# Optimization experiments

Measured on AMD Instinct MI355X. Metric: run time of the kernel, lower is better.

## Reference

```python
import jax, jax.numpy as jnp
import numpy as np

C, KT, D, De, Df, H, PH = 2048, 64, 1024, 128, 256, 8, 1024


def setup_inputs() -> dict:
    key = jax.random.key(0)
    ks = jax.random.split(key, 10)
    wscale = lambda k, shape: jax.random.normal(k, shape, jnp.float32) * 0.02
    return {
        "w": jax.random.normal(ks[0], (C, D), jnp.float32),
        "F": jax.random.normal(ks[1], (C, KT, D), jnp.float32),
        "Et": jax.random.normal(ks[2], (C, KT, De), jnp.float32),
        "fC": jax.random.normal(ks[3], (C, Df), jnp.float32),
        "W1": wscale(ks[4], (D, D + De)),   # K proj (out, in), Linear weight layout
        "W2": wscale(ks[5], (D, D)),        # Q proj
        "Wv": wscale(ks[6], (D, D + De)),   # V proj
        "Wf": wscale(ks[7], (D, Df)),       # fC_proj
        "alpha": jnp.full((1,), 0.1, jnp.float32),
        "beta": jnp.full((1,), 0.1, jnp.float32),
        "g1_w": wscale(ks[8], (PH, D + De)),
        "g1_b": jnp.zeros((PH,), jnp.float32),
        "g2_w": wscale(ks[9], (D, PH)),
        "g2_b": jnp.full((D,), -2.0, jnp.float32),  # bias init fill_(-2.0)
    }


def reference(w, F, Et, fC, W1, W2, Wv, Wf, alpha, beta, g1_w, g1_b, g2_w, g2_b):
    Cc, KTt, Dd = F.shape
    Hh = H
    dh = Dd // Hh
    Fp = jnp.concatenate([F, Et], axis=-1)                 # [C,KT,D+De]
    K = jnp.einsum('ckx,dx->ckd', Fp, W1)                  # [C,KT,D]
    Q = w @ W2.T                                           # [C,D]
    V = jnp.einsum('ckx,dx->ckd', Fp, Wv)                  # [C,KT,D]
    fCp = fC @ Wf.T                                        # [C,D]
    K = K + alpha * fCp[:, None, :]
    Q = Q + beta * fCp
    Qh = Q.reshape(Cc, Hh, dh)                             # [C,H,dh]
    Kh = K.reshape(Cc, KTt, Hh, dh)                        # [C,KT,H,dh]
    Vh = V.reshape(Cc, KTt, Hh, dh)
    scores = jnp.einsum('chd,ckhd->chk', Qh, Kh) / jnp.sqrt(jnp.float32(dh))
    attn = jax.nn.softmax(scores, axis=-1)                 # [C,H,KT]
    A = jnp.einsum('chk,ckhd->chd', attn, Vh).reshape(Cc, Dd)
    gin = jnp.concatenate([w, Et.mean(axis=1)], axis=-1)   # [C,D+De]
    hmid = jax.nn.relu(gin @ g1_w.T + g1_b)
    g = jax.nn.sigmoid(hmid @ g2_w.T + g2_b)               # [C,D] (vec_gate)
    out = w + g * A
    norm = jnp.linalg.norm(out, axis=-1, keepdims=True)
    return out / jnp.maximum(norm, 1e-12)
```

## Files before the change

### kernel.cpp

```cpp
#include <hip/hip_runtime.h>


#define DEV __device__ __forceinline__

typedef __attribute__((ext_vector_type(4))) float f32x4;
typedef __attribute__((ext_vector_type(8))) short bf16x8;
typedef __attribute__((ext_vector_type(4))) unsigned short u16x4;

DEV unsigned short f2b(float f) {
  unsigned int u = __builtin_bit_cast(unsigned int, f);
  u = u + 0x7fffu + ((u >> 16) & 1u);
  return (unsigned short)(u >> 16);
}

enum { MQ = 0, MQT = 1, MAP = 2, MG1 = 3, MG2 = 4 };

template <int MODE>
__global__ __launch_bounds__(256) void gemm64(
    const float* __restrict__ A1, const float* __restrict__ A2,
    const unsigned short* __restrict__ Ab,
    const float* __restrict__ B1, const float* __restrict__ B2,
    const float* __restrict__ scale2, const float* __restrict__ bias,
    float* __restrict__ OutF, unsigned short* __restrict__ OutB)
{
  __shared__ unsigned short As[64 * 40];
  __shared__ unsigned short Bs[64 * 40];

  const int tid = threadIdx.x;
  const int lane = tid & 63, wv = tid >> 6;
  const int l15 = lane & 15, s = lane >> 4;
  const int bx = blockIdx.x, by = blockIdx.y, h = blockIdx.z;
  const int c0 = by * 64;
  const int n0 = bx * 64;

  int K;
  if constexpr (MODE == MQ) K = 1280;
  else if constexpr (MODE == MQT) K = 128;
  else if constexpr (MODE == MAP) K = 1152;
  else if constexpr (MODE == MG1) K = 1152;
  else K = 1024;

  float s2 = 1.0f;
  if constexpr (MODE == MQ) s2 = scale2[0];

  f32x4 acc[4] = {};

  for (int k0 = 0; k0 < K; k0 += 32) {
    if constexpr (MODE == MQ || MODE == MG1) {
      #pragma unroll
      for (int p = 0; p < 2; ++p) {
        int flat = tid + 256 * p;
        int r = flat >> 3, kc = (flat & 7) * 4;
        int k = k0 + kc;
        float4 v;
        if constexpr (MODE == MQ) {
          if (k < 1024) v = *(const float4*)(A1 + (size_t)(c0 + r) * 1024 + k);
          else {
            v = *(const float4*)(A2 + (size_t)(c0 + r) * 256 + (k - 1024));
            v.x *= s2; v.y *= s2; v.z *= s2; v.w *= s2;
          }
        } else {
          if (k < 1024) v = *(const float4*)(A1 + (size_t)(c0 + r) * 1024 + k);
          else v = *(const float4*)(A2 + (size_t)(c0 + r) * 128 + (k - 1024));
        }
        unsigned short* dst = As + r * 40 + kc;
        dst[0] = f2b(v.x); dst[1] = f2b(v.y); dst[2] = f2b(v.z); dst[3] = f2b(v.w);
      }
    } else {
      int r = tid >> 2, kc = (tid & 3) * 8;
      size_t lda, aoff;
      if constexpr (MODE == MQT)      { lda = 1024; aoff = (size_t)h * 128; }
      else if constexpr (MODE == MAP) { lda = 9216; aoff = (size_t)h * 1152; }
      else                            { lda = 1024; aoff = 0; }
      bf16x8 v = *(const bf16x8*)(Ab + (size_t)(c0 + r) * lda + aoff + k0 + kc);
      *(bf16x8*)(As + r * 40 + kc) = v;
    }
    if constexpr (MODE == MQT) {
      #pragma unroll
      for (int p = 0; p < 8; ++p) {
        int flat = tid + 256 * p;
        int kk = flat >> 6, nn = flat & 63;
        float v = B1[(size_t)(h * 128 + k0 + kk) * 1152 + n0 + nn];
        Bs[nn * 40 + kk] = f2b(v);
      }
    } else {
      #pragma unroll
      for (int p = 0; p < 2; ++p) {
        int flat = tid + 256 * p;
        int nn = flat >> 3, kc = (flat & 7) * 4;
        int k = k0 + kc;
        float4 v;
        if constexpr (MODE == MQ) {
          if (k < 1024) v = *(const float4*)(B1 + (size_t)(n0 + nn) * 1024 + k);
          else v = *(const float4*)(B2 + (size_t)(n0 + nn) * 256 + (k - 1024));
        } else if constexpr (MODE == MAP) {
          v = *(const float4*)(B1 + (size_t)(h * 128 + n0 + nn) * 1152 + k);
        } else if constexpr (MODE == MG1) {
          v = *(const float4*)(B1 + (size_t)(n0 + nn) * 1152 + k);
        } else {
          v = *(const float4*)(B1 + (size_t)(n0 + nn) * 1024 + k);
        }
        unsigned short* dst = Bs + nn * 40 + kc;
        dst[0] = f2b(v.x); dst[1] = f2b(v.y); dst[2] = f2b(v.z); dst[3] = f2b(v.w);
      }
    }
    __syncthreads();
    bf16x8 bF = *(const bf16x8*)(Bs + (wv * 16 + l15) * 40 + s * 8);
    #pragma unroll
    for (int ms = 0; ms < 4; ++ms) {
      bf16x8 aF = *(const bf16x8*)(As + (ms * 16 + l15) * 40 + s * 8);
      acc[ms] = __builtin_amdgcn_mfma_f32_16x16x32_bf16(aF, bF, acc[ms], 0, 0, 0);
    }
    __syncthreads();
  }

  #pragma unroll
  for (int ms = 0; ms < 4; ++ms) {
    #pragma unroll
    for (int r = 0; r < 4; ++r) {
      int row = c0 + ms * 16 + s * 4 + r;
      int col = n0 + wv * 16 + l15;
      float v = acc[ms][r];
      if constexpr (MODE == MQ) {
        OutB[(size_t)row * 1024 + col] = f2b(v);
      } else if constexpr (MODE == MQT) {
        OutB[(size_t)row * 9216 + h * 1152 + col] = f2b(v);
      } else if constexpr (MODE == MAP) {
        OutF[(size_t)row * 1024 + h * 128 + col] = v;
      } else if constexpr (MODE == MG1) {
        v += bias[col];
        v = fmaxf(v, 0.0f);
        OutB[(size_t)row * 1024 + col] = f2b(v);
      } else {
        v += bias[col];
        v = 1.0f / (1.0f + __expf(-v));
        OutF[(size_t)row * 1024 + col] = v;
      }
    }
  }
}

__global__ __launch_bounds__(512) void attn_kern(
    const float* __restrict__ F, const float* __restrict__ Et,
    const unsigned short* __restrict__ Qtb,
    unsigned short* __restrict__ Pb, float* __restrict__ Etm)
{
  extern __shared__ char smem[];
  unsigned short* fp = (unsigned short*)smem;
  float* sc = (float*)(smem + (size_t)64 * 1160 * 2);

  const int c = blockIdx.x;
  const int tid = threadIdx.x;
  const int wv = tid >> 6, lane = tid & 63;
  const int l15 = lane & 15, s = lane >> 4;

  const float* Fc = F + (size_t)c * (64 * 1024);
  const float* Ec = Et + (size_t)c * (64 * 128);

  #pragma unroll 4
  for (int j = 0; j < 36; ++j) {
    int i = tid + 512 * j;
    int row = i / 288;
    int c4 = (i % 288) * 4;
    float4 v;
    if (c4 < 1024) v = *(const float4*)(Fc + (size_t)row * 1024 + c4);
    else           v = *(const float4*)(Ec + (size_t)row * 128 + (c4 - 1024));
    u16x4 t4 = { f2b(v.x), f2b(v.y), f2b(v.z), f2b(v.w) };
    *(u16x4*)(fp + (size_t)row * 1160 + c4) = t4;
  }
  __syncthreads();

  if (wv < 4) {
    f32x4 acc = {};
    const unsigned short* qrow = Qtb + ((size_t)c * 8 + l15) * 1152 + s * 8;
    const unsigned short* frow = fp + (size_t)(wv * 16 + l15) * 1160 + s * 8;
    #pragma unroll 4
    for (int x0 = 0; x0 < 1152; x0 += 32) {
      bf16x8 aF = {};
      if (l15 < 8) aF = *(const bf16x8*)(qrow + x0);
      bf16x8 bF = *(const bf16x8*)(frow + x0);
      acc = __builtin_amdgcn_mfma_f32_16x16x32_bf16(aF, bF, acc, 0, 0, 0);
    }
    if (s < 2) {
      #pragma unroll
      for (int r = 0; r < 4; ++r)
        sc[(s * 4 + r) * 64 + wv * 16 + l15] = acc[r] * 0.08838834764831845f;
    }
  } else {
    int u = tid - 256;
    if (u < 128) {
      float ssum = 0.f;
      #pragma unroll 8
      for (int k = 0; k < 64; ++k) ssum += Ec[(size_t)k * 128 + u];
      Etm[(size_t)c * 128 + u] = ssum * (1.0f / 64.0f);
    }
  }
  __syncthreads();

  {
    float sv = sc[wv * 64 + lane];
    float m = sv;
    #pragma unroll
    for (int off = 32; off; off >>= 1) m = fmaxf(m, __shfl_xor(m, off));
    float e = __expf(sv - m);
    float sum = e;
    #pragma unroll
    for (int off = 32; off; off >>= 1) sum += __shfl_xor(sum, off);
    sc[wv * 64 + lane] = e / sum;
  }
  __syncthreads();

  bf16x8 pa[2];
  #pragma unroll
  for (int ki = 0; ki < 2; ++ki) {
    bf16x8 t = {};
    if (l15 < 8) {
      #pragma unroll
      for (int j = 0; j < 8; ++j)
        t[j] = (short)f2b(sc[l15 * 64 + ki * 32 + j * 4 + s]);
    }
    pa[ki] = t;
  }
  #pragma unroll
  for (int ntl = 0; ntl < 9; ++ntl) {
    int nt = wv * 9 + ntl;
    int x = nt * 16 + l15;
    f32x4 acc = {};
    #pragma unroll
    for (int ki = 0; ki < 2; ++ki) {
      bf16x8 bF;
      #pragma unroll
      for (int j = 0; j < 8; ++j)
        bF[j] = (short)fp[(size_t)(ki * 32 + j * 4 + s) * 1160 + x];
      acc = __builtin_amdgcn_mfma_f32_16x16x32_bf16(pa[ki], bF, acc, 0, 0, 0);
    }
    if (s < 2) {
      #pragma unroll
      for (int r = 0; r < 4; ++r) {
        int hh = s * 4 + r;
        Pb[((size_t)c * 8 + hh) * 1152 + x] = f2b(acc[r]);
      }
    }
  }
}

__global__ __launch_bounds__(256) void finalize_kern(
    const float* __restrict__ w, const float* __restrict__ A,
    const float* __restrict__ g, float* __restrict__ out)
{
  __shared__ float red[4];
  int c = blockIdx.x, t = threadIdx.x;
  int lane = t & 63, wid = t >> 6;
  size_t base = (size_t)c * 1024 + t * 4;
  float4 wv = *(const float4*)(w + base);
  float4 av = *(const float4*)(A + base);
  float4 gv = *(const float4*)(g + base);
  float4 o;
  o.x = wv.x + gv.x * av.x;
  o.y = wv.y + gv.y * av.y;
  o.z = wv.z + gv.z * av.z;
  o.w = wv.w + gv.w * av.w;
  float ss = o.x * o.x + o.y * o.y + o.z * o.z + o.w * o.w;
  #pragma unroll
  for (int off = 32; off; off >>= 1) ss += __shfl_xor(ss, off);
  if (lane == 0) red[wid] = ss;
  __syncthreads();
  float tot = red[0] + red[1] + red[2] + red[3];
  float inv = 1.0f / fmaxf(sqrtf(tot), 1e-12f);
  o.x *= inv; o.y *= inv; o.z *= inv; o.w *= inv;
  *(float4*)(out + base) = o;
}

extern "C" void kernel_launch(void* const* d_in, const int* in_sizes, int n_in,
                              void* d_out, int out_size, void* d_ws, size_t ws_size,
                              hipStream_t stream)
{
  (void)in_sizes; (void)n_in; (void)out_size; (void)ws_size;
  const float* w    = (const float*)d_in[0];
  const float* F    = (const float*)d_in[1];
  const float* Et   = (const float*)d_in[2];
  const float* fC   = (const float*)d_in[3];
  const float* W1   = (const float*)d_in[4];
  const float* W2   = (const float*)d_in[5];
  const float* Wv   = (const float*)d_in[6];
  const float* Wf   = (const float*)d_in[7];
  const float* beta = (const float*)d_in[9];
  const float* g1w  = (const float*)d_in[10];
  const float* g1b  = (const float*)d_in[11];
  const float* g2w  = (const float*)d_in[12];
  const float* g2b  = (const float*)d_in[13];
  float* outp = (float*)d_out;

  char* ws = (char*)d_ws;
  unsigned short* Qb  = (unsigned short*)(ws + 0);
  unsigned short* Qtb = (unsigned short*)(ws + 4194304);
  unsigned short* Pb  = (unsigned short*)(ws + 41943040);
  float* Etm          = (float*)(ws + 79691776);
  float* Afp          = (float*)(ws + 80740352);
  unsigned short* Hm  = (unsigned short*)(ws + 4194304);
  float* Gf           = (float*)(ws + 0);

  gemm64<MQ><<<dim3(16, 32), 256, 0, stream>>>(w, fC, nullptr, W2, Wf, beta,
                                               nullptr, nullptr, Qb);
  gemm64<MQT><<<dim3(18, 32, 8), 256, 0, stream>>>(nullptr, nullptr, Qb, W1,
                                                   nullptr, nullptr, nullptr,
                                                   nullptr, Qtb);
  attn_kern<<<2048, 512, 150528, stream>>>(F, Et, Qtb, Pb, Etm);
  gemm64<MAP><<<dim3(2, 32, 8), 256, 0, stream>>>(nullptr, nullptr, Pb, Wv,
                                                  nullptr, nullptr, nullptr,
                                                  Afp, nullptr);
  gemm64<MG1><<<dim3(16, 32), 256, 0, stream>>>(w, Etm, nullptr, g1w, nullptr,
                                                nullptr, g1b, nullptr, Hm);
  gemm64<MG2><<<dim3(16, 32), 256, 0, stream>>>(nullptr, nullptr, Hm, g2w,
                                                nullptr, nullptr, g2b, Gf,
                                                nullptr);
  finalize_kern<<<2048, 256, 0, stream>>>(w, Afp, Gf, outp);
}
```

Before: 1.250 ms.

## Stream attention tiles via async LDS loads with online softmax; widen GEMM K-tile with swizzle

The attention kernel now streams F and Et in four 16-row tiles using global_load_lds into double-buffered fp32 LDS with XOR swizzle. It splits the score reduction across all 8 waves and uses an online softmax with running max and sum rescaling. This is meant to overlap global loads with MFMA work and drop the up-front bulk conversion pass. Separately, the GEMM kernels move to a 64-wide K step with swizzled LDS rows to cut bank conflicts and halve the barrier count. The costs are more LDS (156800 bytes, which rules out two blocks per CU despite the launch bound), per-tile bf16 conversion during compute, and extra synchronization per tile.

```diff
diff --git a/kernel.cpp b/kernel.cpp
--- a/kernel.cpp
+++ b/kernel.cpp
@@ -12,6 +12,26 @@
   u = u + 0x7fffu + ((u >> 16) & 1u);
   return (unsigned short)(u >> 16);
 }
+
+DEV bf16x8 cvt8(f32x4 a, f32x4 b) {
+  bf16x8 r;
+  r[0] = (short)f2b(a[0]); r[1] = (short)f2b(a[1]);
+  r[2] = (short)f2b(a[2]); r[3] = (short)f2b(a[3]);
+  r[4] = (short)f2b(b[0]); r[5] = (short)f2b(b[1]);
+  r[6] = (short)f2b(b[2]); r[7] = (short)f2b(b[3]);
+  return r;
+}
+
+DEV void gll16(const void* g, void* l) {
+  __builtin_amdgcn_global_load_lds(
+      (const __attribute__((address_space(1))) void*)g,
+      (__attribute__((address_space(3))) void*)l, 16, 0, 0);
+}
+
+#define SBAR0() __builtin_amdgcn_sched_barrier(0)
+#define LGKM_BARRIER() do { \
+    asm volatile("s_waitcnt lgkmcnt(0)" ::: "memory"); \
+    SBAR0(); __builtin_amdgcn_s_barrier(); SBAR0(); } while (0)
 
 enum { MQ = 0, MQT = 1, MAP = 2, MG1 = 3, MG2 = 4 };
 
@@ -23,8 +43,8 @@
     const float* __restrict__ scale2, const float* __restrict__ bias,
     float* __restrict__ OutF, unsigned short* __restrict__ OutB)
 {
-  __shared__ unsigned short As[64 * 40];
-  __shared__ unsigned short Bs[64 * 40];
+  __shared__ unsigned short As[64 * 64];
+  __shared__ unsigned short Bs[64 * 64];
 
   const int tid = threadIdx.x;
   const int lane = tid & 63, wv = tid >> 6;
@@ -45,12 +65,12 @@
 
   f32x4 acc[4] = {};
 
-  for (int k0 = 0; k0 < K; k0 += 32) {
+  for (int k0 = 0; k0 < K; k0 += 64) {
     if constexpr (MODE == MQ || MODE == MG1) {
       #pragma unroll
-      for (int p = 0; p < 2; ++p) {
+      for (int p = 0; p < 4; ++p) {
         int flat = tid + 256 * p;
-        int r = flat >> 3, kc = (flat & 7) * 4;
+        int r = flat >> 4, kc = (flat & 15) * 4;
         int k = k0 + kc;
         float4 v;
         if constexpr (MODE == MQ) {
@@ -63,31 +83,35 @@
           if (k < 1024) v = *(const float4*)(A1 + (size_t)(c0 + r) * 1024 + k);
           else v = *(const float4*)(A2 + (size_t)(c0 + r) * 128 + (k - 1024));
         }
-        unsigned short* dst = As + r * 40 + kc;
-        dst[0] = f2b(v.x); dst[1] = f2b(v.y); dst[2] = f2b(v.z); dst[3] = f2b(v.w);
+        u16x4 t4 = { f2b(v.x), f2b(v.y), f2b(v.z), f2b(v.w) };
+        *(u16x4*)((char*)As + r * 128 + ((kc * 2) ^ ((r & 7) << 4))) = t4;
       }
     } else {
-      int r = tid >> 2, kc = (tid & 3) * 8;
-      size_t lda, aoff;
-      if constexpr (MODE == MQT)      { lda = 1024; aoff = (size_t)h * 128; }
-      else if constexpr (MODE == MAP) { lda = 9216; aoff = (size_t)h * 1152; }
-      else                            { lda = 1024; aoff = 0; }
-      bf16x8 v = *(const bf16x8*)(Ab + (size_t)(c0 + r) * lda + aoff + k0 + kc);
-      *(bf16x8*)(As + r * 40 + kc) = v;
+      #pragma unroll
+      for (int p = 0; p < 2; ++p) {
+        int flat = tid + 256 * p;
+        int r = flat >> 3, kc8 = (flat & 7) * 8;
+        size_t lda, aoff;
+        if constexpr (MODE == MQT)      { lda = 1024; aoff = (size_t)h * 128; }
+        else if constexpr (MODE == MAP) { lda = 9216; aoff = (size_t)h * 1152; }
+        else                            { lda = 1024; aoff = 0; }
+        bf16x8 v = *(const bf16x8*)(Ab + (size_t)(c0 + r) * lda + aoff + k0 + kc8);
+        *(bf16x8*)((char*)As + r * 128 + ((kc8 * 2) ^ ((r & 7) << 4))) = v;
+      }
     }
     if constexpr (MODE == MQT) {
       #pragma unroll
-      for (int p = 0; p < 8; ++p) {
+      for (int p = 0; p < 16; ++p) {
         int flat = tid + 256 * p;
         int kk = flat >> 6, nn = flat & 63;
         float v = B1[(size_t)(h * 128 + k0 + kk) * 1152 + n0 + nn];
-        Bs[nn * 40 + kk] = f2b(v);
+        *(unsigned short*)((char*)Bs + nn * 128 + ((kk * 2) ^ ((nn & 7) << 4))) = f2b(v);
       }
     } else {
       #pragma unroll
-      for (int p = 0; p < 2; ++p) {
+      for (int p = 0; p < 4; ++p) {
         int flat = tid + 256 * p;
-        int nn = flat >> 3, kc = (flat & 7) * 4;
+        int nn = flat >> 4, kc = (flat & 15) * 4;
         int k = k0 + kc;
         float4 v;
         if constexpr (MODE == MQ) {
@@ -100,16 +124,21 @@
         } else {
           v = *(const float4*)(B1 + (size_t)(n0 + nn) * 1024 + k);
         }
-        unsigned short* dst = Bs + nn * 40 + kc;
-        dst[0] = f2b(v.x); dst[1] = f2b(v.y); dst[2] = f2b(v.z); dst[3] = f2b(v.w);
+        u16x4 t4 = { f2b(v.x), f2b(v.y), f2b(v.z), f2b(v.w) };
+        *(u16x4*)((char*)Bs + nn * 128 + ((kc * 2) ^ ((nn & 7) << 4))) = t4;
       }
     }
     __syncthreads();
-    bf16x8 bF = *(const bf16x8*)(Bs + (wv * 16 + l15) * 40 + s * 8);
     #pragma unroll
-    for (int ms = 0; ms < 4; ++ms) {
-      bf16x8 aF = *(const bf16x8*)(As + (ms * 16 + l15) * 40 + s * 8);
-      acc[ms] = __builtin_amdgcn_mfma_f32_16x16x32_bf16(aF, bF, acc[ms], 0, 0, 0);
+    for (int kk = 0; kk < 2; ++kk) {
+      bf16x8 bF = *(const bf16x8*)((char*)Bs + (wv * 16 + l15) * 128 +
+                                   ((kk * 64 + s * 16) ^ ((l15 & 7) << 4)));
+      #pragma unroll
+      for (int ms = 0; ms < 4; ++ms) {
+        bf16x8 aF = *(const bf16x8*)((char*)As + (ms * 16 + l15) * 128 +
+                                     ((kk * 64 + s * 16) ^ ((l15 & 7) << 4)));
+        acc[ms] = __builtin_amdgcn_mfma_f32_16x16x32_bf16(aF, bF, acc[ms], 0, 0, 0);
+      }
     }
     __syncthreads();
   }
@@ -140,108 +169,173 @@
   }
 }
 
-__global__ __launch_bounds__(512) void attn_kern(
+#define FT_OFF 0
+#define ET_OFF 131072
+#define PSC_OFF 147456
+#define WL_OFF 155648
+#define ST_OFF 156672
+
+DEV void stage_tile(const float* Fc, const float* Ec, char* FtBuf, char* EtBuf,
+                    int t, int wv, int lane) {
+  const int l16 = lane * 16;
+  #pragma unroll
+  for (int i = 0; i < 8; ++i) {
+    int ci = wv * 8 + i;
+    int r = ci >> 2, q = ci & 3;
+    int swz = (r & 7) << 5;
+    const char* src = (const char*)Fc + (size_t)(t * 16 + r) * 4096 + q * 1024 + (l16 ^ swz);
+    gll16(src, FtBuf + ci * 1024);
+  }
+  {
+    int r = 2 * wv + (lane >> 5);
+    int b = (lane & 31) * 16;
+    int swz = (r & 7) << 5;
+    const char* src = (const char*)Ec + (size_t)(t * 16 + r) * 512 + (b ^ swz);
+    gll16(src, EtBuf + wv * 1024);
+  }
+}
+
+__global__ __launch_bounds__(512, 2) void attn_kern(
     const float* __restrict__ F, const float* __restrict__ Et,
     const unsigned short* __restrict__ Qtb,
     unsigned short* __restrict__ Pb, float* __restrict__ Etm)
 {
   extern __shared__ char smem[];
-  unsigned short* fp = (unsigned short*)smem;
-  float* sc = (float*)(smem + (size_t)64 * 1160 * 2);
+  float* psc = (float*)(smem + PSC_OFF);
+  unsigned short* wl = (unsigned short*)(smem + WL_OFF);
+  float* mrun = (float*)(smem + ST_OFF);
+  float* lrun = mrun + 8;
+  float* rfs  = mrun + 16;
 
   const int c = blockIdx.x;
   const int tid = threadIdx.x;
   const int wv = tid >> 6, lane = tid & 63;
   const int l15 = lane & 15, s = lane >> 4;
 
-  const float* Fc = F + (size_t)c * (64 * 1024);
-  const float* Ec = Et + (size_t)c * (64 * 128);
-
-  #pragma unroll 4
-  for (int j = 0; j < 36; ++j) {
-    int i = tid + 512 * j;
-    int row = i / 288;
-    int c4 = (i % 288) * 4;
-    float4 v;
-    if (c4 < 1024) v = *(const float4*)(Fc + (size_t)row * 1024 + c4);
-    else           v = *(const float4*)(Ec + (size_t)row * 128 + (c4 - 1024));
-    u16x4 t4 = { f2b(v.x), f2b(v.y), f2b(v.z), f2b(v.w) };
-    *(u16x4*)(fp + (size_t)row * 1160 + c4) = t4;
-  }
-  __syncthreads();
-
-  if (wv < 4) {
-    f32x4 acc = {};
-    const unsigned short* qrow = Qtb + ((size_t)c * 8 + l15) * 1152 + s * 8;
-    const unsigned short* frow = fp + (size_t)(wv * 16 + l15) * 1160 + s * 8;
-    #pragma unroll 4
-    for (int x0 = 0; x0 < 1152; x0 += 32) {
-      bf16x8 aF = {};
-      if (l15 < 8) aF = *(const bf16x8*)(qrow + x0);
-      bf16x8 bF = *(const bf16x8*)(frow + x0);
-      acc = __builtin_amdgcn_mfma_f32_16x16x32_bf16(aF, bF, acc, 0, 0, 0);
-    }
-    if (s < 2) {
-      #pragma unroll
-      for (int r = 0; r < 4; ++r)
-        sc[(s * 4 + r) * 64 + wv * 16 + l15] = acc[r] * 0.08838834764831845f;
-    }
-  } else {
-    int u = tid - 256;
-    if (u < 128) {
-      float ssum = 0.f;
-      #pragma unroll 8
-      for (int k = 0; k < 64; ++k) ssum += Ec[(size_t)k * 128 + u];
-      Etm[(size_t)c * 128 + u] = ssum * (1.0f / 64.0f);
-    }
-  }
-  __syncthreads();
-
-  {
-    float sv = sc[wv * 64 + lane];
-    float m = sv;
+  const float* Fc = F + (size_t)c * 65536;
+  const float* Ec = Et + (size_t)c * 8192;
+
+  wl[tid] = 0;
+  if (tid < 8) { mrun[tid] = -1e30f; lrun[tid] = 0.0f; rfs[tid] = 0.0f; }
+
+  stage_tile(Fc, Ec, smem + FT_OFF, smem + ET_OFF, 0, wv, lane);
+
+  const int nk  = (wv < 4) ? 5 : 4;
+  const int xk0 = (wv < 4) ? wv * 160 : 640 + (wv - 4) * 128;
+  bf16x8 qf[5];
+  #pragma unroll
+  for (int i = 0; i < 5; ++i) { bf16x8 z = {}; qf[i] = z; }
+  if (l15 < 8) {
+    const unsigned short* qp = Qtb + ((size_t)c * 8 + l15) * 1152 + xk0 + s * 8;
     #pragma unroll
-    for (int off = 32; off; off >>= 1) m = fmaxf(m, __shfl_xor(m, off));
-    float e = __expf(sv - m);
-    float sum = e;
+    for (int i = 0; i < 5; ++i) if (i < nk) qf[i] = *(const bf16x8*)(qp + i * 32);
+  }
+
+  f32x4 pacc[9];
+  #pragma unroll
+  for (int i = 0; i < 9; ++i) { f32x4 z = {}; pacc[i] = z; }
+  float etacc = 0.0f;
+
+  for (int t = 0; t < 4; ++t) {
+    char* Fcur = smem + FT_OFF + (t & 1) * 65536;
+    char* Ecur = smem + ET_OFF + (t & 1) * 8192;
+
+    __syncthreads();
+    if (t < 3)
+      stage_tile(Fc, Ec, smem + FT_OFF + ((t + 1) & 1) * 65536,
+                 smem + ET_OFF + ((t + 1) & 1) * 8192, t + 1, wv, lane);
+    SBAR0();
+
+    {
+      f32x4 sa = {};
+      #pragma unroll
+      for (int i = 0; i < 5; ++i) {
+        if (i < nk) {
+          int xk = xk0 + i * 32;
+          const char* base; int off;
+          if (xk < 1024) { base = Fcur; off = l15 * 4096 + ((xk * 4 + s * 32) ^ ((l15 & 7) << 5)); }
+          else           { base = Ecur; off = l15 * 512  + (((xk - 1024) * 4 + s * 32) ^ ((l15 & 7) << 5)); }
+          f32x4 u0 = *(const f32x4*)(base + off);
+          f32x4 u1 = *(const f32x4*)(base + off + 16);
+          sa = __builtin_amdgcn_mfma_f32_16x16x32_bf16(qf[i], cvt8(u0, u1), sa, 0, 0, 0);
+        }
+      }
+      *(f32x4*)(psc + wv * 256 + l15 * 16 + s * 4) = sa;
+    }
+    LGKM_BARRIER();
+
+    if (tid < 128) {
+      int hh = tid >> 4, j = tid & 15;
+      float sv = 0.0f;
+      #pragma unroll
+      for (int w2 = 0; w2 < 8; ++w2) sv += psc[w2 * 256 + j * 16 + hh];
+      sv *= 0.08838834764831845f;
+      float mt = sv;
+      #pragma unroll
+      for (int o = 8; o; o >>= 1) mt = fmaxf(mt, __shfl_xor(mt, o));
+      float mo = mrun[hh];
+      float mn = fmaxf(mo, mt);
+      float e = __expf(sv - mn);
+      float lt = e;
+      #pragma unroll
+      for (int o = 8; o; o >>= 1) lt += __shfl_xor(lt, o);
+      float rf = __expf(mo - mn);
+      wl[hh * 32 + j] = f2b(e);
+      if (j == 0) { mrun[hh] = mn; lrun[hh] = lrun[hh] * rf + lt; rfs[hh] = rf; }
+    } else if (tid < 256) {
+      int u = tid - 128;
+      float a = 0.0f;
+      #pragma unroll
+      for (int r = 0; r < 16; ++r)
+        a += *(const float*)(Ecur + r * 512 + ((u * 4) ^ ((r & 7) << 5)));
+      etacc += a;
+    }
+    LGKM_BARRIER();
+
+    {
+      bf16x8 pa0 = *(const bf16x8*)((const char*)wl + l15 * 64 + s * 16);
+      float rfv[4];
+      #pragma unroll
+      for (int r = 0; r < 4; ++r) rfv[r] = rfs[(s * 4 + r) & 7];
+      #pragma unroll
+      for (int i = 0; i < 9; ++i) {
+        #pragma unroll
+        for (int r = 0; r < 4; ++r) pacc[i][r] *= rfv[r];
+        int ch = wv * 9 + i;
+        int xg = ch * 16 + l15;
+        bf16x8 bf;
+        #pragma unroll
+        for (int j = 0; j < 8; ++j) {
+          float v = 0.0f;
+          if (s < 2) {
+            int k = s * 8 + j;
+            if (ch < 64) v = *(const float*)(Fcur + k * 4096 + ((xg * 4) ^ ((k & 7) << 5)));
+            else         v = *(const float*)(Ecur + k * 512  + (((xg - 1024) * 4) ^ ((k & 7) << 5)));
+          }
+          bf[j] = (short)f2b(v);
+        }
+        pacc[i] = __builtin_amdgcn_mfma_f32_16x16x32_bf16(pa0, bf, pacc[i], 0, 0, 0);
+      }
+    }
+    SBAR0();
+  }
+
+  float rl[4];
+  #pragma unroll
+  for (int r = 0; r < 4; ++r) rl[r] = 1.0f / lrun[(s * 4 + r) & 7];
+  if (s < 2) {
     #pragma unroll
-    for (int off = 32; off; off >>= 1) sum += __shfl_xor(sum, off);
-    sc[wv * 64 + lane] = e / sum;
-  }
-  __syncthreads();
-
-  bf16x8 pa[2];
-  #pragma unroll
-  for (int ki = 0; ki < 2; ++ki) {
-    bf16x8 t = {};
-    if (l15 < 8) {
-      #pragma unroll
-      for (int j = 0; j < 8; ++j)
-        t[j] = (short)f2b(sc[l15 * 64 + ki * 32 + j * 4 + s]);
-    }
-    pa[ki] = t;
-  }
-  #pragma unroll
-  for (int ntl = 0; ntl < 9; ++ntl) {
-    int nt = wv * 9 + ntl;
-    int x = nt * 16 + l15;
-    f32x4 acc = {};
-    #pragma unroll
-    for (int ki = 0; ki < 2; ++ki) {
-      bf16x8 bF;
-      #pragma unroll
-      for (int j = 0; j < 8; ++j)
-        bF[j] = (short)fp[(size_t)(ki * 32 + j * 4 + s) * 1160 + x];
-      acc = __builtin_amdgcn_mfma_f32_16x16x32_bf16(pa[ki], bF, acc, 0, 0, 0);
-    }
-    if (s < 2) {
+    for (int i = 0; i < 9; ++i) {
+      int xg = (wv * 9 + i) * 16 + l15;
       #pragma unroll
       for (int r = 0; r < 4; ++r) {
         int hh = s * 4 + r;
-        Pb[((size_t)c * 8 + hh) * 1152 + x] = f2b(acc[r]);
-      }
-    }
-  }
+        Pb[((size_t)c * 8 + hh) * 1152 + xg] = f2b(pacc[i][r] * rl[r]);
+      }
+    }
+  }
+  if (tid >= 128 && tid < 256)
+    Etm[(size_t)c * 128 + (tid - 128)] = etacc * (1.0f / 64.0f);
 }
 
 __global__ __launch_bounds__(256) void finalize_kern(
@@ -305,7 +399,7 @@
   gemm64<MQT><<<dim3(18, 32, 8), 256, 0, stream>>>(nullptr, nullptr, Qb, W1,
                                                    nullptr, nullptr, nullptr,
                                                    nullptr, Qtb);
-  attn_kern<<<2048, 512, 150528, stream>>>(F, Et, Qtb, Pb, Etm);
+  attn_kern<<<2048, 512, 156800, stream>>>(F, Et, Qtb, Pb, Etm);
   gemm64<MAP><<<dim3(2, 32, 8), 256, 0, stream>>>(nullptr, nullptr, Pb, Wv,
                                                   nullptr, nullptr, nullptr,
                                                   Afp, nullptr);
```

Result: faster. 1.116 ms (-10.7%).
